# Optimization experiments

Hardware: AMD Instinct MI355X
Metric: run time of the kernel (lower is better)

Reference implementation:

```python
import jax, jax.numpy as jnp
import numpy as np
import math

B, T, VOCAB, RANK = 32, 1024, 512, 256


def setup_inputs() -> dict:
    key = jax.random.key(0)
    k1, k2, k3, k4, k5 = jax.random.split(key, 5)
    scale_attn = 1.0 / math.sqrt(VOCAB)
    scale_proj = 1.0 / math.sqrt(RANK)
    return {
        "x": jax.random.normal(k1, (B, T, VOCAB), dtype=jnp.float32),
        "W_attn": jax.random.normal(k2, (VOCAB, 3 * RANK), dtype=jnp.float32) * scale_attn,
        "b_attn": jax.random.normal(k3, (3 * RANK,), dtype=jnp.float32) * 0.01,
        "W_proj": jax.random.normal(k4, (RANK, VOCAB), dtype=jnp.float32) * scale_proj,
        "b_proj": jax.random.normal(k5, (VOCAB,), dtype=jnp.float32) * 0.01,
    }


def reference(x, W_attn, b_attn, W_proj, b_proj):
    # x: [B, T, vocab]
    Bb, Tt, _ = x.shape
    qkv = x @ W_attn + b_attn              # [B, T, 3*rank]
    q, k, v = jnp.split(qkv, 3, axis=-1)   # each [B, T, rank]
    scale = 1.0 / math.sqrt(k.shape[-1])
    att = jnp.einsum('btd,bsd->bts', q, k) * scale  # [B, T, T]
    # causal mask (masked=True)
    mask = jnp.tril(jnp.ones((Tt, Tt), dtype=bool))
    att = jnp.where(mask[None, :, :], att, -jnp.inf)
    att = jax.nn.softmax(att, axis=-1)
    # dropout layers are identity in eval mode (p=0 attn, p=0.1 resid disabled)
    y = jnp.einsum('bts,bsd->btd', att, v)  # [B, T, rank]
    y = y @ W_proj + b_proj                 # [B, T, vocab]
    return jax.nn.gelu(y, approximate=False)
```

## Files before the change

kernel.cpp:

```cpp
#include <hip/hip_runtime.h>
#include <hip/hip_bf16.h>
#include <math.h>

typedef __bf16 bf16;
typedef __attribute__((ext_vector_type(8))) __bf16 bf16x8;
typedef __attribute__((ext_vector_type(4))) __bf16 bf16x4;
typedef __attribute__((ext_vector_type(4))) float f32x4;

#define MFMA16(a, b, c) __builtin_amdgcn_mfma_f32_16x16x32_bf16((a), (b), (c), 0, 0, 0)


__global__ __launch_bounds__(256) void cvt_w(const float* __restrict__ wa,
                                             const float* __restrict__ wp,
                                             bf16* __restrict__ wt1,
                                             bf16* __restrict__ wt2) {
  int o = blockIdx.x * 256 + threadIdx.x;
  if (o < 393216) {
    int n = o >> 9, kk = o & 511;
    wt1[o] = (bf16)wa[kk * 768 + n];
  } else {
    int o2 = o - 393216;
    int n = o2 >> 8, kk = o2 & 255;
    wt2[o2] = (bf16)wp[kk * 512 + n];
  }
}

__global__ __launch_bounds__(256) void gemm_qkv(
    const float* __restrict__ x, const bf16* __restrict__ WT,
    const float* __restrict__ b_attn,
    bf16* __restrict__ qo, bf16* __restrict__ ko, bf16* __restrict__ vto) {
  __shared__ __attribute__((aligned(16))) bf16 As[128][40];
  __shared__ __attribute__((aligned(16))) bf16 Bs[128][40];
  const int tid = threadIdx.x;
  const int id = blockIdx.x;
  const int xcd = id & 7;
  const int rest = id >> 3;
  const int bmL = rest / 6;
  const int bn = (rest % 6) * 128;
  const int bm = (xcd * 32 + bmL) * 128;
  const int lane = tid & 63, wid = tid >> 6;
  const int l15 = lane & 15, lg = lane >> 4;
  const int wm = (wid >> 1) * 64, wn = (wid & 1) * 64;

  f32x4 acc[4][4] = {};

  const int srow = tid >> 1;
  const int scol = (tid & 1) * 16;
  const float* xp = x + (size_t)(bm + srow) * 512 + scol;
  const bf16* wp = WT + (size_t)(bn + srow) * 512 + scol;

  bf16x8 ha[2], hb[2];
  {
    f32x4 f0 = *(const f32x4*)(xp);
    f32x4 f1 = *(const f32x4*)(xp + 4);
    f32x4 f2 = *(const f32x4*)(xp + 8);
    f32x4 f3 = *(const f32x4*)(xp + 12);
#pragma unroll
    for (int e = 0; e < 4; ++e) {
      ha[0][e] = (bf16)f0[e]; ha[0][e + 4] = (bf16)f1[e];
      ha[1][e] = (bf16)f2[e]; ha[1][e + 4] = (bf16)f3[e];
    }
    hb[0] = *(const bf16x8*)(wp);
    hb[1] = *(const bf16x8*)(wp + 8);
  }

  for (int kt = 0; kt < 16; ++kt) {
    __syncthreads();
    *(bf16x8*)&As[srow][scol] = ha[0];
    *(bf16x8*)&As[srow][scol + 8] = ha[1];
    *(bf16x8*)&Bs[srow][scol] = hb[0];
    *(bf16x8*)&Bs[srow][scol + 8] = hb[1];
    __syncthreads();
    if (kt < 15) {
      f32x4 f0 = *(const f32x4*)(xp + (kt + 1) * 32);
      f32x4 f1 = *(const f32x4*)(xp + (kt + 1) * 32 + 4);
      f32x4 f2 = *(const f32x4*)(xp + (kt + 1) * 32 + 8);
      f32x4 f3 = *(const f32x4*)(xp + (kt + 1) * 32 + 12);
#pragma unroll
      for (int e = 0; e < 4; ++e) {
        ha[0][e] = (bf16)f0[e]; ha[0][e + 4] = (bf16)f1[e];
        ha[1][e] = (bf16)f2[e]; ha[1][e + 4] = (bf16)f3[e];
      }
      hb[0] = *(const bf16x8*)(wp + (kt + 1) * 32);
      hb[1] = *(const bf16x8*)(wp + (kt + 1) * 32 + 8);
    }
    bf16x8 af[4], bfr[4];
#pragma unroll
    for (int mi = 0; mi < 4; ++mi)
      af[mi] = *(const bf16x8*)&As[wm + mi * 16 + l15][lg * 8];
#pragma unroll
    for (int ni = 0; ni < 4; ++ni)
      bfr[ni] = *(const bf16x8*)&Bs[wn + ni * 16 + l15][lg * 8];
    __builtin_amdgcn_s_setprio(1);
#pragma unroll
    for (int mi = 0; mi < 4; ++mi)
#pragma unroll
      for (int ni = 0; ni < 4; ++ni)
        acc[mi][ni] = MFMA16(bfr[ni], af[mi], acc[mi][ni]);
    __builtin_amdgcn_s_setprio(0);
  }

#pragma unroll
  for (int ni = 0; ni < 4; ++ni) {
    int gc0 = bn + wn + ni * 16 + lg * 4;
    f32x4 bias = *(const f32x4*)(b_attn + gc0);
    int seg = gc0 >> 8;
    int cc = gc0 & 255;
    if (seg == 2) {
#pragma unroll
      for (int mi = 0; mi < 4; ++mi) {
        int gr = bm + wm + mi * 16 + l15;
        bf16* vp = vto + (size_t)(gr >> 10) * 262144 + (size_t)cc * 1024 + (gr & 1023);
#pragma unroll
        for (int r = 0; r < 4; ++r)
          vp[(size_t)r * 1024] = (bf16)(acc[mi][ni][r] + bias[r]);
      }
    } else {
      bf16* op = (seg == 0) ? qo : ko;
#pragma unroll
      for (int mi = 0; mi < 4; ++mi) {
        int gr = bm + wm + mi * 16 + l15;
        bf16x4 pk;
#pragma unroll
        for (int r = 0; r < 4; ++r) pk[r] = (bf16)(acc[mi][ni][r] + bias[r]);
        *(bf16x4*)(op + (size_t)gr * 256 + cc) = pk;
      }
    }
  }
}

__global__ __launch_bounds__(256) void attn_fwd(
    const bf16* __restrict__ q, const bf16* __restrict__ k,
    const bf16* __restrict__ vt, bf16* __restrict__ y) {
  __shared__ __attribute__((aligned(16))) bf16 Ks[64 * 256];
  __shared__ __attribute__((aligned(16))) bf16 Vt[256 * 64];
  __shared__ __attribute__((aligned(16))) bf16 Ps[4 * 16 * 64];
  const int tid = threadIdx.x, lane = tid & 63, wid = tid >> 6;
  const int l15 = lane & 15, lg = lane >> 4;

  const int id = blockIdx.x;
  const int xcd = id & 7, u = id >> 3;
  const int bg = u & 3, j = u >> 2;
  const int b = xcd + 8 * bg;
  const int qt = (j < 8) ? j : 23 - j;
  const int q0 = qt * 64 + wid * 16;

  bf16x8 qf[8];
  {
    const bf16* qp = q + (size_t)(b * 1024 + q0 + l15) * 256 + lg * 8;
#pragma unroll
    for (int d = 0; d < 8; ++d) qf[d] = *(const bf16x8*)(qp + d * 32);
  }
  f32x4 o[16] = {};
  float m_st = -1e30f;
  float l_st = 0.f;

  const char* kbase = (const char*)(k + (size_t)b * 262144);
  const char* vtbase = (const char*)(vt + (size_t)b * 262144);
  const int ksr = tid >> 5;
  const int kscb = (tid & 31) * 16;
  const int kkey = ksr << 4;
  const int vsr = tid >> 3;
  const int vscb = (tid & 7) * 16;
  const int vkey = (vsr & 7) << 4;
  const int rkey = (l15 & 7) << 4;

  const int ntiles = qt + 1;

  bf16x8 kreg[8], vreg[8];
#pragma unroll
  for (int i = 0; i < 8; ++i)
    kreg[i] = *(const bf16x8*)(kbase + (size_t)(ksr + i * 8) * 512 + kscb);
#pragma unroll
  for (int i = 0; i < 8; ++i)
    vreg[i] = *(const bf16x8*)(vtbase + (size_t)(vsr + i * 32) * 2048 + vscb);

  for (int tt = 0; tt < ntiles; ++tt) {
    const int kv0 = tt * 64;
    __syncthreads();
#pragma unroll
    for (int i = 0; i < 8; ++i)
      *(bf16x8*)((char*)Ks + (size_t)(ksr + i * 8) * 512 + (kscb ^ kkey)) = kreg[i];
#pragma unroll
    for (int i = 0; i < 8; ++i)
      *(bf16x8*)((char*)Vt + (size_t)(vsr + i * 32) * 128 + (vscb ^ vkey)) = vreg[i];
    __syncthreads();
    if (tt + 1 < ntiles) {
      const char* kp = kbase + (size_t)(kv0 + 64) * 512;
      const char* vp = vtbase + (size_t)(kv0 + 64) * 2;
#pragma unroll
      for (int i = 0; i < 8; ++i)
        kreg[i] = *(const bf16x8*)(kp + (size_t)(ksr + i * 8) * 512 + kscb);
#pragma unroll
      for (int i = 0; i < 8; ++i)
        vreg[i] = *(const bf16x8*)(vp + (size_t)(vsr + i * 32) * 2048 + vscb);
    }

    f32x4 st[4] = {};
    __builtin_amdgcn_s_setprio(1);
#pragma unroll
    for (int nf = 0; nf < 4; ++nf) {
      const char* rp = (const char*)Ks + (size_t)(nf * 16 + l15) * 512;
#pragma unroll
      for (int dc = 0; dc < 8; ++dc) {
        bf16x8 kb = *(const bf16x8*)(rp + ((dc * 64 + lg * 16) ^ rkey));
        st[nf] = MFMA16(kb, qf[dc], st[nf]);
      }
    }
    __builtin_amdgcn_s_setprio(0);

    const int qg = q0 + l15;
    float tmax = -1e30f;
#pragma unroll
    for (int nf = 0; nf < 4; ++nf)
#pragma unroll
      for (int r = 0; r < 4; ++r) {
        int sg = kv0 + nf * 16 + lg * 4 + r;
        float v = st[nf][r] * 0.0625f;
        v = (sg > qg) ? -1e30f : v;
        st[nf][r] = v;
        tmax = fmaxf(tmax, v);
      }
    tmax = fmaxf(tmax, __shfl_xor(tmax, 16, 64));
    tmax = fmaxf(tmax, __shfl_xor(tmax, 32, 64));

    if (!__all(tmax <= m_st + 8.f)) {
      float mnew = fmaxf(m_st, tmax);
      float corr = __expf(m_st - mnew);
      m_st = mnew;
      l_st *= corr;
#pragma unroll
      for (int df = 0; df < 16; ++df)
#pragma unroll
        for (int r = 0; r < 4; ++r) o[df][r] *= corr;
    }

    char* psw = (char*)Ps + wid * 2048 + l15 * 128;
    float rsum = 0.f;
#pragma unroll
    for (int nf = 0; nf < 4; ++nf) {
      bf16x4 pk;
#pragma unroll
      for (int r = 0; r < 4; ++r) {
        float p = __expf(st[nf][r] - m_st);
        rsum += p;
        pk[r] = (bf16)p;
      }
      *(bf16x4*)(psw + ((nf * 32 + lg * 8) ^ rkey)) = pk;
    }
    rsum += __shfl_xor(rsum, 16, 64);
    rsum += __shfl_xor(rsum, 32, 64);
    l_st += rsum;

    bf16x8 pa0 = *(const bf16x8*)(psw + ((lg * 16) ^ rkey));
    bf16x8 pa1 = *(const bf16x8*)(psw + ((64 + lg * 16) ^ rkey));
    __builtin_amdgcn_s_setprio(1);
#pragma unroll
    for (int df = 0; df < 16; ++df) {
      const char* rp = (const char*)Vt + (size_t)(df * 16 + l15) * 128;
      bf16x8 vb0 = *(const bf16x8*)(rp + ((lg * 16) ^ rkey));
      bf16x8 vb1 = *(const bf16x8*)(rp + ((64 + lg * 16) ^ rkey));
      o[df] = MFMA16(vb0, pa0, o[df]);
      o[df] = MFMA16(vb1, pa1, o[df]);
    }
    __builtin_amdgcn_s_setprio(0);
  }

  float inv = 1.f / l_st;
  bf16* yp = y + (size_t)(b * 1024 + q0 + l15) * 256 + lg * 4;
#pragma unroll
  for (int df = 0; df < 16; ++df) {
    bf16x4 pk;
#pragma unroll
    for (int r = 0; r < 4; ++r) pk[r] = (bf16)(o[df][r] * inv);
    *(bf16x4*)(yp + df * 16) = pk;
  }
}

__global__ __launch_bounds__(256) void gemm_proj(
    const bf16* __restrict__ y, const bf16* __restrict__ WT,
    const float* __restrict__ b_proj, float* __restrict__ out) {
  __shared__ __attribute__((aligned(16))) bf16 As[128][40];
  __shared__ __attribute__((aligned(16))) bf16 Bs[128][40];
  const int tid = threadIdx.x;
  const int id = blockIdx.x;
  const int xcd = id & 7;
  const int rest = id >> 3;
  const int bmL = rest >> 2;
  const int bn = (rest & 3) * 128;
  const int bm = (xcd * 32 + bmL) * 128;
  const int lane = tid & 63, wid = tid >> 6;
  const int l15 = lane & 15, lg = lane >> 4;
  const int wm = (wid >> 1) * 64, wn = (wid & 1) * 64;
  f32x4 acc[4][4] = {};

  const int srow = tid >> 1, scol = (tid & 1) * 16;
  const bf16* yp = y + (size_t)(bm + srow) * 256 + scol;
  const bf16* wp = WT + (size_t)(bn + srow) * 256 + scol;

  bf16x8 ha[2], hb[2];
  ha[0] = *(const bf16x8*)(yp);
  ha[1] = *(const bf16x8*)(yp + 8);
  hb[0] = *(const bf16x8*)(wp);
  hb[1] = *(const bf16x8*)(wp + 8);

  for (int kt = 0; kt < 8; ++kt) {
    __syncthreads();
    *(bf16x8*)&As[srow][scol] = ha[0];  *(bf16x8*)&As[srow][scol + 8] = ha[1];
    *(bf16x8*)&Bs[srow][scol] = hb[0];  *(bf16x8*)&Bs[srow][scol + 8] = hb[1];
    __syncthreads();
    if (kt < 7) {
      ha[0] = *(const bf16x8*)(yp + (kt + 1) * 32);
      ha[1] = *(const bf16x8*)(yp + (kt + 1) * 32 + 8);
      hb[0] = *(const bf16x8*)(wp + (kt + 1) * 32);
      hb[1] = *(const bf16x8*)(wp + (kt + 1) * 32 + 8);
    }
    bf16x8 af[4], bfr[4];
#pragma unroll
    for (int mi = 0; mi < 4; ++mi)
      af[mi] = *(const bf16x8*)&As[wm + mi * 16 + l15][lg * 8];
#pragma unroll
    for (int ni = 0; ni < 4; ++ni)
      bfr[ni] = *(const bf16x8*)&Bs[wn + ni * 16 + l15][lg * 8];
    __builtin_amdgcn_s_setprio(1);
#pragma unroll
    for (int mi = 0; mi < 4; ++mi)
#pragma unroll
      for (int ni = 0; ni < 4; ++ni)
        acc[mi][ni] = MFMA16(bfr[ni], af[mi], acc[mi][ni]);
    __builtin_amdgcn_s_setprio(0);
  }

#pragma unroll
  for (int ni = 0; ni < 4; ++ni) {
    int gc0 = bn + wn + ni * 16 + lg * 4;
    f32x4 bias = *(const f32x4*)(b_proj + gc0);
#pragma unroll
    for (int mi = 0; mi < 4; ++mi) {
      int gr = bm + wm + mi * 16 + l15;
      f32x4 g;
#pragma unroll
      for (int r = 0; r < 4; ++r) {
        float v = acc[mi][ni][r] + bias[r];
        float z = 1.5957691216f * (v + 0.044715f * v * v * v);
        float t = __expf(z);
        float th = 1.f - 2.f / (t + 1.f);
        g[r] = 0.5f * v * (1.f + th);
      }
      *(f32x4*)(out + (size_t)gr * 512 + gc0) = g;
    }
  }
}

extern "C" void kernel_launch(void* const* d_in, const int* in_sizes, int n_in,
                              void* d_out, int out_size, void* d_ws, size_t ws_size,
                              hipStream_t stream) {
  const float* x      = (const float*)d_in[0];
  const float* W_attn = (const float*)d_in[1];
  const float* b_attn = (const float*)d_in[2];
  const float* W_proj = (const float*)d_in[3];
  const float* b_proj = (const float*)d_in[4];
  float* out = (float*)d_out;
  char* ws = (char*)d_ws;

  const size_t SZ = 16777216;
  bf16* WT1 = (bf16*)(ws);
  bf16* WT2 = (bf16*)(ws + 786432);
  bf16* qb  = (bf16*)(ws + 1048576);
  bf16* kb  = (bf16*)(ws + 1048576 + SZ);
  bf16* vtb = (bf16*)(ws + 1048576 + 2 * SZ);
  bf16* yb  = (bf16*)(ws + 1048576 + 3 * SZ);

  cvt_w<<<dim3(2048), dim3(256), 0, stream>>>(W_attn, W_proj, WT1, WT2);
  gemm_qkv<<<dim3(1536), dim3(256), 0, stream>>>(x, WT1, b_attn, qb, kb, vtb);
  attn_fwd<<<dim3(512), dim3(256), 0, stream>>>(qb, kb, vtb, yb);
  gemm_proj<<<dim3(1024), dim3(256), 0, stream>>>(yb, WT2, b_proj, out);
}
```

Measured before the change: 132.7 us.

## Pre-convert x to bf16 and use double-buffered global_load_lds in GEMMs

Adds a separate cvt_x kernel that converts x from fp32 to bf16 into a workspace buffer, so gemm_qkv reads bf16 instead of converting fp32 inline. Both GEMMs replace register-staged global loads plus LDS stores with direct global-to-LDS loads into a double-buffered, unpadded LDS tile, with one barrier per k-step. The goal is to overlap tile fetches with MFMA work and cut staging instructions. In exchange it adds an extra full pass over x (read fp32, write bf16, read again). The unpadded LDS rows may also cause bank conflicts on fragment reads. The bf16 x buffer aliases the y buffer region and needs more bytes than y occupies.

```diff
diff --git a/kernel.cpp b/kernel.cpp
--- a/kernel.cpp
+++ b/kernel.cpp
@@ -8,6 +8,12 @@
 typedef __attribute__((ext_vector_type(4))) float f32x4;
 
 #define MFMA16(a, b, c) __builtin_amdgcn_mfma_f32_16x16x32_bf16((a), (b), (c), 0, 0, 0)
+
+__device__ __forceinline__ void glds16(const bf16* g, bf16* l) {
+  __builtin_amdgcn_global_load_lds(
+      (const __attribute__((address_space(1))) unsigned int*)g,
+      (__attribute__((address_space(3))) unsigned int*)l, 16, 0, 0);
+}
 
 
 __global__ __launch_bounds__(256) void cvt_w(const float* __restrict__ wa,
@@ -25,12 +31,23 @@
   }
 }
 
+__global__ __launch_bounds__(256) void cvt_x(const float* __restrict__ x,
+                                             bf16* __restrict__ xb) {
+  size_t i = ((size_t)blockIdx.x * 256 + threadIdx.x) * 8;
+  f32x4 f0 = *(const f32x4*)(x + i);
+  f32x4 f1 = *(const f32x4*)(x + i + 4);
+  bf16x8 h;
+#pragma unroll
+  for (int e = 0; e < 4; ++e) { h[e] = (bf16)f0[e]; h[e + 4] = (bf16)f1[e]; }
+  *(bf16x8*)(xb + i) = h;
+}
+
 __global__ __launch_bounds__(256) void gemm_qkv(
-    const float* __restrict__ x, const bf16* __restrict__ WT,
+    const bf16* __restrict__ xb, const bf16* __restrict__ WT,
     const float* __restrict__ b_attn,
     bf16* __restrict__ qo, bf16* __restrict__ ko, bf16* __restrict__ vto) {
-  __shared__ __attribute__((aligned(16))) bf16 As[128][40];
-  __shared__ __attribute__((aligned(16))) bf16 Bs[128][40];
+  __shared__ __attribute__((aligned(16))) bf16 As[2][128][32];
+  __shared__ __attribute__((aligned(16))) bf16 Bs[2][128][32];
   const int tid = threadIdx.x;
   const int id = blockIdx.x;
   const int xcd = id & 7;
@@ -44,53 +61,39 @@
 
   f32x4 acc[4][4] = {};
 
-  const int srow = tid >> 1;
-  const int scol = (tid & 1) * 16;
-  const float* xp = x + (size_t)(bm + srow) * 512 + scol;
-  const bf16* wp = WT + (size_t)(bn + srow) * 512 + scol;
-
-  bf16x8 ha[2], hb[2];
+  const int ar = tid >> 2;
+  const int ac = (tid & 3) * 8;
+  const bf16* aB = xb + (size_t)(bm + ar) * 512 + ac;
+  const bf16* bB = WT + (size_t)(bn + ar) * 512 + ac;
+
   {
-    f32x4 f0 = *(const f32x4*)(xp);
-    f32x4 f1 = *(const f32x4*)(xp + 4);
-    f32x4 f2 = *(const f32x4*)(xp + 8);
-    f32x4 f3 = *(const f32x4*)(xp + 12);
-#pragma unroll
-    for (int e = 0; e < 4; ++e) {
-      ha[0][e] = (bf16)f0[e]; ha[0][e + 4] = (bf16)f1[e];
-      ha[1][e] = (bf16)f2[e]; ha[1][e + 4] = (bf16)f3[e];
-    }
-    hb[0] = *(const bf16x8*)(wp);
-    hb[1] = *(const bf16x8*)(wp + 8);
-  }
-
+    bf16* A0 = &As[0][0][0];
+    bf16* B0 = &Bs[0][0][0];
+    glds16(aB,            A0 + (size_t)tid * 8);
+    glds16(aB + 64 * 512, A0 + (size_t)(256 + tid) * 8);
+    glds16(bB,            B0 + (size_t)tid * 8);
+    glds16(bB + 64 * 512, B0 + (size_t)(256 + tid) * 8);
+  }
+  __syncthreads();
+
+  int cur = 0;
   for (int kt = 0; kt < 16; ++kt) {
-    __syncthreads();
-    *(bf16x8*)&As[srow][scol] = ha[0];
-    *(bf16x8*)&As[srow][scol + 8] = ha[1];
-    *(bf16x8*)&Bs[srow][scol] = hb[0];
-    *(bf16x8*)&Bs[srow][scol + 8] = hb[1];
-    __syncthreads();
     if (kt < 15) {
-      f32x4 f0 = *(const f32x4*)(xp + (kt + 1) * 32);
-      f32x4 f1 = *(const f32x4*)(xp + (kt + 1) * 32 + 4);
-      f32x4 f2 = *(const f32x4*)(xp + (kt + 1) * 32 + 8);
-      f32x4 f3 = *(const f32x4*)(xp + (kt + 1) * 32 + 12);
-#pragma unroll
-      for (int e = 0; e < 4; ++e) {
-        ha[0][e] = (bf16)f0[e]; ha[0][e + 4] = (bf16)f1[e];
-        ha[1][e] = (bf16)f2[e]; ha[1][e + 4] = (bf16)f3[e];
-      }
-      hb[0] = *(const bf16x8*)(wp + (kt + 1) * 32);
-      hb[1] = *(const bf16x8*)(wp + (kt + 1) * 32 + 8);
+      const int k0 = (kt + 1) * 32;
+      bf16* An = &As[cur ^ 1][0][0];
+      bf16* Bn = &Bs[cur ^ 1][0][0];
+      glds16(aB + k0,            An + (size_t)tid * 8);
+      glds16(aB + 64 * 512 + k0, An + (size_t)(256 + tid) * 8);
+      glds16(bB + k0,            Bn + (size_t)tid * 8);
+      glds16(bB + 64 * 512 + k0, Bn + (size_t)(256 + tid) * 8);
     }
     bf16x8 af[4], bfr[4];
 #pragma unroll
     for (int mi = 0; mi < 4; ++mi)
-      af[mi] = *(const bf16x8*)&As[wm + mi * 16 + l15][lg * 8];
+      af[mi] = *(const bf16x8*)&As[cur][wm + mi * 16 + l15][lg * 8];
 #pragma unroll
     for (int ni = 0; ni < 4; ++ni)
-      bfr[ni] = *(const bf16x8*)&Bs[wn + ni * 16 + l15][lg * 8];
+      bfr[ni] = *(const bf16x8*)&Bs[cur][wn + ni * 16 + l15][lg * 8];
     __builtin_amdgcn_s_setprio(1);
 #pragma unroll
     for (int mi = 0; mi < 4; ++mi)
@@ -98,6 +101,8 @@
       for (int ni = 0; ni < 4; ++ni)
         acc[mi][ni] = MFMA16(bfr[ni], af[mi], acc[mi][ni]);
     __builtin_amdgcn_s_setprio(0);
+    __syncthreads();
+    cur ^= 1;
   }
 
 #pragma unroll
@@ -280,8 +285,8 @@
 __global__ __launch_bounds__(256) void gemm_proj(
     const bf16* __restrict__ y, const bf16* __restrict__ WT,
     const float* __restrict__ b_proj, float* __restrict__ out) {
-  __shared__ __attribute__((aligned(16))) bf16 As[128][40];
-  __shared__ __attribute__((aligned(16))) bf16 Bs[128][40];
+  __shared__ __attribute__((aligned(16))) bf16 As[2][128][32];
+  __shared__ __attribute__((aligned(16))) bf16 Bs[2][128][32];
   const int tid = threadIdx.x;
   const int id = blockIdx.x;
   const int xcd = id & 7;
@@ -294,34 +299,39 @@
   const int wm = (wid >> 1) * 64, wn = (wid & 1) * 64;
   f32x4 acc[4][4] = {};
 
-  const int srow = tid >> 1, scol = (tid & 1) * 16;
-  const bf16* yp = y + (size_t)(bm + srow) * 256 + scol;
-  const bf16* wp = WT + (size_t)(bn + srow) * 256 + scol;
-
-  bf16x8 ha[2], hb[2];
-  ha[0] = *(const bf16x8*)(yp);
-  ha[1] = *(const bf16x8*)(yp + 8);
-  hb[0] = *(const bf16x8*)(wp);
-  hb[1] = *(const bf16x8*)(wp + 8);
-
+  const int ar = tid >> 2;
+  const int ac = (tid & 3) * 8;
+  const bf16* aB = y + (size_t)(bm + ar) * 256 + ac;
+  const bf16* bB = WT + (size_t)(bn + ar) * 256 + ac;
+
+  {
+    bf16* A0 = &As[0][0][0];
+    bf16* B0 = &Bs[0][0][0];
+    glds16(aB,            A0 + (size_t)tid * 8);
+    glds16(aB + 64 * 256, A0 + (size_t)(256 + tid) * 8);
+    glds16(bB,            B0 + (size_t)tid * 8);
+    glds16(bB + 64 * 256, B0 + (size_t)(256 + tid) * 8);
+  }
+  __syncthreads();
+
+  int cur = 0;
   for (int kt = 0; kt < 8; ++kt) {
-    __syncthreads();
-    *(bf16x8*)&As[srow][scol] = ha[0];  *(bf16x8*)&As[srow][scol + 8] = ha[1];
-    *(bf16x8*)&Bs[srow][scol] = hb[0];  *(bf16x8*)&Bs[srow][scol + 8] = hb[1];
-    __syncthreads();
     if (kt < 7) {
-      ha[0] = *(const bf16x8*)(yp + (kt + 1) * 32);
-      ha[1] = *(const bf16x8*)(yp + (kt + 1) * 32 + 8);
-      hb[0] = *(const bf16x8*)(wp + (kt + 1) * 32);
-      hb[1] = *(const bf16x8*)(wp + (kt + 1) * 32 + 8);
+      const int k0 = (kt + 1) * 32;
+      bf16* An = &As[cur ^ 1][0][0];
+      bf16* Bn = &Bs[cur ^ 1][0][0];
+      glds16(aB + k0,            An + (size_t)tid * 8);
+      glds16(aB + 64 * 256 + k0, An + (size_t)(256 + tid) * 8);
+      glds16(bB + k0,            Bn + (size_t)tid * 8);
+      glds16(bB + 64 * 256 + k0, Bn + (size_t)(256 + tid) * 8);
     }
     bf16x8 af[4], bfr[4];
 #pragma unroll
     for (int mi = 0; mi < 4; ++mi)
-      af[mi] = *(const bf16x8*)&As[wm + mi * 16 + l15][lg * 8];
+      af[mi] = *(const bf16x8*)&As[cur][wm + mi * 16 + l15][lg * 8];
 #pragma unroll
     for (int ni = 0; ni < 4; ++ni)
-      bfr[ni] = *(const bf16x8*)&Bs[wn + ni * 16 + l15][lg * 8];
+      bfr[ni] = *(const bf16x8*)&Bs[cur][wn + ni * 16 + l15][lg * 8];
     __builtin_amdgcn_s_setprio(1);
 #pragma unroll
     for (int mi = 0; mi < 4; ++mi)
@@ -329,6 +339,8 @@
       for (int ni = 0; ni < 4; ++ni)
         acc[mi][ni] = MFMA16(bfr[ni], af[mi], acc[mi][ni]);
     __builtin_amdgcn_s_setprio(0);
+    __syncthreads();
+    cur ^= 1;
   }
 
 #pragma unroll
@@ -370,9 +382,11 @@
   bf16* kb  = (bf16*)(ws + 1048576 + SZ);
   bf16* vtb = (bf16*)(ws + 1048576 + 2 * SZ);
   bf16* yb  = (bf16*)(ws + 1048576 + 3 * SZ);
+  bf16* xbb = (bf16*)(ws + 1048576 + 3 * SZ);
 
   cvt_w<<<dim3(2048), dim3(256), 0, stream>>>(W_attn, W_proj, WT1, WT2);
-  gemm_qkv<<<dim3(1536), dim3(256), 0, stream>>>(x, WT1, b_attn, qb, kb, vtb);
+  cvt_x<<<dim3(8192), dim3(256), 0, stream>>>(x, xbb);
+  gemm_qkv<<<dim3(1536), dim3(256), 0, stream>>>(xbb, WT1, b_attn, qb, kb, vtb);
   attn_fwd<<<dim3(512), dim3(256), 0, stream>>>(qb, kb, vtb, yb);
   gemm_proj<<<dim3(1024), dim3(256), 0, stream>>>(yb, WT2, b_proj, out);
 }
```

Result: slower. 139.7 us (+5.3%).
